# Performance work log

Hardware: AMD Instinct MI355X
Metric: run time of the kernel (lower is better)

## Reference

```python
import jax, jax.numpy as jnp
import numpy as np

N_DATA = 500000
FEAT_DIM = 128
BATCH = 512
N_NEG = 4096
TEMPERATURE = 0.07
MOMENTUM = 0.5
EPS = 1e-12


def _l2norm(x, axis=-1):
    # F.normalize(x, dim): x / max(||x||, eps)
    n = jnp.sqrt(jnp.sum(x * x, axis=axis, keepdims=True))
    return x / jnp.maximum(n, EPS)


def setup_inputs() -> dict:
    key = jax.random.key(0)
    k1, k2, k3, k4, k5 = jax.random.split(key, 5)
    student_feat = jax.random.normal(k1, (BATCH, FEAT_DIM), dtype=jnp.float32)
    teacher_feat = jax.random.normal(k2, (BATCH, FEAT_DIM), dtype=jnp.float32)
    # buffer initialized as normalized gaussian rows (as in __init__)
    memory_bank = _l2norm(jax.random.normal(k3, (N_DATA, FEAT_DIM), dtype=jnp.float32))
    indices = jax.random.randint(k4, (BATCH,), 0, N_DATA, dtype=jnp.int64 if jax.config.jax_enable_x64 else jnp.int32)
    neg_indices = jax.random.randint(k5, (BATCH, N_NEG), 0, N_DATA, dtype=jnp.int64 if jax.config.jax_enable_x64 else jnp.int32)
    return {
        "student_feat": student_feat,
        "teacher_feat": teacher_feat,
        "memory_bank": memory_bank,
        "indices": indices,
        "neg_indices": neg_indices,
    }


def reference(student_feat, teacher_feat, memory_bank, indices, neg_indices):
    s = _l2norm(student_feat)           # [B, D]
    t = _l2norm(teacher_feat)           # [B, D]

    # positive logits: elementwise dot of paired student/teacher rows
    pos_logits = jnp.sum(s * t, axis=1, keepdims=True) / TEMPERATURE   # [B, 1]

    # gather negatives from memory bank, then batched dot products
    neg_feat = memory_bank[neg_indices]                                # [B, K, D]
    neg_logits = jnp.einsum("bd,bkd->bk", s, neg_feat) / TEMPERATURE   # [B, K]

    logits = jnp.concatenate([pos_logits, neg_logits], axis=1)         # [B, 1+K]
    # cross_entropy with label 0 for every row
    loss = jnp.mean(jax.nn.logsumexp(logits, axis=1) - logits[:, 0])

    # momentum scatter-update of the memory bank (no_grad in torch)
    updated = MOMENTUM * memory_bank[indices] + (1.0 - MOMENTUM) * t   # [B, D]
    updated = _l2norm(updated)
    new_memory_bank = memory_bank.at[indices].set(updated)

    return loss, new_memory_bank
```

## Files before the change

### kernel.cpp

```cpp
#include <hip/hip_runtime.h>
#include <cmath>

#define B_SZ 512
#define D_SZ 128
#define K_SZ 4096
#define NDATA 500000
#define TEMP 0.07f
#define MOM 0.5f
#define EPSN 1e-12f
#define SPLIT 8
#define WSB_OFF (1 << 20)

typedef float f32x4 __attribute__((ext_vector_type(4)));
typedef float f32x2 __attribute__((ext_vector_type(2)));

__global__ void knorm(const float* __restrict__ s_in, const float* __restrict__ t_in,
                      float* __restrict__ s_n, float* __restrict__ t_n,
                      float* __restrict__ pos) {
    int b = blockIdx.x;
    int l = threadIdx.x;
    float2 sv = ((const float2*)(s_in + b * D_SZ))[l];
    float2 tv = ((const float2*)(t_in + b * D_SZ))[l];
    float ss = sv.x * sv.x + sv.y * sv.y;
    float tt = tv.x * tv.x + tv.y * tv.y;
    for (int m = 1; m < 64; m <<= 1) {
        ss += __shfl_xor(ss, m, 64);
        tt += __shfl_xor(tt, m, 64);
    }
    float sinv = 1.0f / fmaxf(sqrtf(ss), EPSN);
    float tinv = 1.0f / fmaxf(sqrtf(tt), EPSN);
    float2 sn = {sv.x * sinv, sv.y * sinv};
    float2 tn = {tv.x * tinv, tv.y * tinv};
    ((float2*)(s_n + b * D_SZ))[l] = sn;
    ((float2*)(t_n + b * D_SZ))[l] = tn;
    float d = sn.x * tn.x + sn.y * tn.y;
    for (int m = 1; m < 64; m <<= 1) d += __shfl_xor(d, m, 64);
    if (l == 0) pos[b] = d * (1.0f / TEMP);
}

__global__ __launch_bounds__(256) void kcopy_emit(const float* __restrict__ src,
                                                  float* __restrict__ out ,
                                                  unsigned int* __restrict__ wsb) {
    const long long total = (long long)NDATA * D_SZ;
    const long long NV = total / 4;
    long long t = blockIdx.x * 256LL + threadIdx.x;
    const long long nthr = gridDim.x * 256LL;
    const int lane = threadIdx.x & 63;
    const f32x4* src4 = (const f32x4*)src;
    f32x4* out4 = (f32x4*)out;
    for (long long j = t; j < NV; j += nthr) {
        f32x4 v = __builtin_nontemporal_load(src4 + j);
        int w8 = __builtin_amdgcn_cvt_pk_fp8_f32(v.x, v.y, 0, false);
        w8 = __builtin_amdgcn_cvt_pk_fp8_f32(v.z, v.w, w8, true);
        wsb[j] = (unsigned int)w8;
        float pw = __shfl_up(v.w, 1, 64);
        if (lane == 0 && j > 0) pw = src[4 * j - 1];
        if (j > 0) {
            f32x4 w;
            w.x = pw; w.y = v.x; w.z = v.y; w.w = v.z;
            __builtin_nontemporal_store(w, out4 + j);
        } else {
            out[1] = v.x; out[2] = v.y; out[3] = v.z;
            out[total] = src[total - 1];
        }
    }
}

__global__ __launch_bounds__(256) void kneg_fp8(const unsigned int* __restrict__ wsb,
                                                const int* __restrict__ negidx,
                                                const float* __restrict__ s_n,
                                                float2* __restrict__ partials) {
    const int split = blockIdx.x;
    const int b = blockIdx.y;
    const int tid = threadIdx.x;
    const int oct = tid >> 3;
    const int o = tid & 7;
    const f32x4* sn4 = (const f32x4*)(s_n + b * D_SZ + o * 16);
    f32x4 s0 = sn4[0], s1 = sn4[1], s2 = sn4[2], s3 = sn4[3];
    float m = -INFINITY, ssum = 0.0f;
    const int KB = K_SZ / SPLIT;
    const int base = b * K_SZ + split * KB;
    for (int it = 0; it < KB / 128; ++it) {
        int k = it * 128 + oct * 4;
        int4 idx = *(const int4*)(negidx + base + k);
        uint4 h0 = ((const uint4*)(wsb + (long long)idx.x * 32))[o];
        uint4 h1 = ((const uint4*)(wsb + (long long)idx.y * 32))[o];
        uint4 h2 = ((const uint4*)(wsb + (long long)idx.z * 32))[o];
        uint4 h3 = ((const uint4*)(wsb + (long long)idx.w * 32))[o];
        float d0 = 0.0f, d1 = 0.0f, d2 = 0.0f, d3 = 0.0f;
        {
            f32x2 a, c;
            a = __builtin_amdgcn_cvt_pk_f32_fp8((int)h0.x, false);
            c = __builtin_amdgcn_cvt_pk_f32_fp8((int)h0.x, true);
            d0 += a.x * s0.x + a.y * s0.y + c.x * s0.z + c.y * s0.w;
            a = __builtin_amdgcn_cvt_pk_f32_fp8((int)h0.y, false);
            c = __builtin_amdgcn_cvt_pk_f32_fp8((int)h0.y, true);
            d0 += a.x * s1.x + a.y * s1.y + c.x * s1.z + c.y * s1.w;
            a = __builtin_amdgcn_cvt_pk_f32_fp8((int)h0.z, false);
            c = __builtin_amdgcn_cvt_pk_f32_fp8((int)h0.z, true);
            d0 += a.x * s2.x + a.y * s2.y + c.x * s2.z + c.y * s2.w;
            a = __builtin_amdgcn_cvt_pk_f32_fp8((int)h0.w, false);
            c = __builtin_amdgcn_cvt_pk_f32_fp8((int)h0.w, true);
            d0 += a.x * s3.x + a.y * s3.y + c.x * s3.z + c.y * s3.w;

            a = __builtin_amdgcn_cvt_pk_f32_fp8((int)h1.x, false);
            c = __builtin_amdgcn_cvt_pk_f32_fp8((int)h1.x, true);
            d1 += a.x * s0.x + a.y * s0.y + c.x * s0.z + c.y * s0.w;
            a = __builtin_amdgcn_cvt_pk_f32_fp8((int)h1.y, false);
            c = __builtin_amdgcn_cvt_pk_f32_fp8((int)h1.y, true);
            d1 += a.x * s1.x + a.y * s1.y + c.x * s1.z + c.y * s1.w;
            a = __builtin_amdgcn_cvt_pk_f32_fp8((int)h1.z, false);
            c = __builtin_amdgcn_cvt_pk_f32_fp8((int)h1.z, true);
            d1 += a.x * s2.x + a.y * s2.y + c.x * s2.z + c.y * s2.w;
            a = __builtin_amdgcn_cvt_pk_f32_fp8((int)h1.w, false);
            c = __builtin_amdgcn_cvt_pk_f32_fp8((int)h1.w, true);
            d1 += a.x * s3.x + a.y * s3.y + c.x * s3.z + c.y * s3.w;

            a = __builtin_amdgcn_cvt_pk_f32_fp8((int)h2.x, false);
            c = __builtin_amdgcn_cvt_pk_f32_fp8((int)h2.x, true);
            d2 += a.x * s0.x + a.y * s0.y + c.x * s0.z + c.y * s0.w;
            a = __builtin_amdgcn_cvt_pk_f32_fp8((int)h2.y, false);
            c = __builtin_amdgcn_cvt_pk_f32_fp8((int)h2.y, true);
            d2 += a.x * s1.x + a.y * s1.y + c.x * s1.z + c.y * s1.w;
            a = __builtin_amdgcn_cvt_pk_f32_fp8((int)h2.z, false);
            c = __builtin_amdgcn_cvt_pk_f32_fp8((int)h2.z, true);
            d2 += a.x * s2.x + a.y * s2.y + c.x * s2.z + c.y * s2.w;
            a = __builtin_amdgcn_cvt_pk_f32_fp8((int)h2.w, false);
            c = __builtin_amdgcn_cvt_pk_f32_fp8((int)h2.w, true);
            d2 += a.x * s3.x + a.y * s3.y + c.x * s3.z + c.y * s3.w;

            a = __builtin_amdgcn_cvt_pk_f32_fp8((int)h3.x, false);
            c = __builtin_amdgcn_cvt_pk_f32_fp8((int)h3.x, true);
            d3 += a.x * s0.x + a.y * s0.y + c.x * s0.z + c.y * s0.w;
            a = __builtin_amdgcn_cvt_pk_f32_fp8((int)h3.y, false);
            c = __builtin_amdgcn_cvt_pk_f32_fp8((int)h3.y, true);
            d3 += a.x * s1.x + a.y * s1.y + c.x * s1.z + c.y * s1.w;
            a = __builtin_amdgcn_cvt_pk_f32_fp8((int)h3.z, false);
            c = __builtin_amdgcn_cvt_pk_f32_fp8((int)h3.z, true);
            d3 += a.x * s2.x + a.y * s2.y + c.x * s2.z + c.y * s2.w;
            a = __builtin_amdgcn_cvt_pk_f32_fp8((int)h3.w, false);
            c = __builtin_amdgcn_cvt_pk_f32_fp8((int)h3.w, true);
            d3 += a.x * s3.x + a.y * s3.y + c.x * s3.z + c.y * s3.w;
        }
        for (int s = 1; s < 8; s <<= 1) {
            d0 += __shfl_xor(d0, s, 64);
            d1 += __shfl_xor(d1, s, 64);
            d2 += __shfl_xor(d2, s, 64);
            d3 += __shfl_xor(d3, s, 64);
        }
        d0 *= (1.0f / TEMP);
        d1 *= (1.0f / TEMP);
        d2 *= (1.0f / TEMP);
        d3 *= (1.0f / TEMP);
        float mx = fmaxf(fmaxf(d0, d1), fmaxf(d2, d3));
        float mn = fmaxf(m, mx);
        ssum = ssum * __expf(m - mn) + __expf(d0 - mn) + __expf(d1 - mn) +
               __expf(d2 - mn) + __expf(d3 - mn);
        m = mn;
    }
    __shared__ float2 gp[32];
    if (o == 0) gp[oct] = make_float2(m, ssum);
    __syncthreads();
    if (tid == 0) {
        float M = gp[0].x, S = gp[0].y;
        for (int g = 1; g < 32; ++g) {
            float mg = gp[g].x, sg = gp[g].y;
            float mn = fmaxf(M, mg);
            S = S * __expf(M - mn) + sg * __expf(mg - mn);
            M = mn;
        }
        partials[b * SPLIT + split] = make_float2(M, S);
    }
}

__global__ void kupdate(const int* __restrict__ indices, const float* __restrict__ bank,
                        const float* __restrict__ t_n, float* __restrict__ outBank ) {
    int j = blockIdx.x;
    int l = threadIdx.x;
    int idx = indices[j];
    for (int j2 = j + 1; j2 < B_SZ; ++j2)
        if (indices[j2] == idx) return;
    float2 bv = ((const float2*)(bank + (long long)idx * D_SZ))[l];
    float2 tv = ((const float2*)(t_n + j * D_SZ))[l];
    float2 u = {MOM * bv.x + (1.0f - MOM) * tv.x, MOM * bv.y + (1.0f - MOM) * tv.y};
    float ss = u.x * u.x + u.y * u.y;
    for (int m = 1; m < 64; m <<= 1) ss += __shfl_xor(ss, m, 64);
    float inv = 1.0f / fmaxf(sqrtf(ss), EPSN);
    float* dst = outBank + (long long)idx * D_SZ + l * 2;
    dst[0] = u.x * inv;
    dst[1] = u.y * inv;
}

__global__ void kfinal(const float2* __restrict__ partials, const float* __restrict__ pos,
                       float* __restrict__ out) {
    __shared__ float red[B_SZ];
    int t = threadIdx.x;
    float M = -INFINITY, S = 0.0f;
    for (int p = 0; p < SPLIT; ++p) {
        float2 ms = partials[t * SPLIT + p];
        float mn = fmaxf(M, ms.x);
        S = S * __expf(M - mn) + ms.y * __expf(ms.x - mn);
        M = mn;
    }
    float pl = pos[t];
    float mn = fmaxf(M, pl);
    S = S * __expf(M - mn) + __expf(pl - mn);
    M = mn;
    red[t] = M + logf(S) - pl;
    __syncthreads();
    for (int off = 256; off > 0; off >>= 1) {
        if (t < off) red[t] += red[t + off];
        __syncthreads();
    }
    if (t == 0) out[0] = red[0] * (1.0f / (float)B_SZ);
}

extern "C" void kernel_launch(void* const* d_in, const int* in_sizes, int n_in,
                              void* d_out, int out_size, void* d_ws, size_t ws_size,
                              hipStream_t stream) {
    const float* student = (const float*)d_in[0];
    const float* teacher = (const float*)d_in[1];
    const float* bank    = (const float*)d_in[2];
    const int*   indices = (const int*)d_in[3];
    const int*   negidx  = (const int*)d_in[4];
    float* out = (float*)d_out;

    float* s_n      = (float*)d_ws;
    float* t_n      = s_n + B_SZ * D_SZ;
    float* pos      = t_n + B_SZ * D_SZ;
    float2* partials = (float2*)(pos + B_SZ);
    unsigned int* wsb = (unsigned int*)((char*)d_ws + WSB_OFF);

    knorm<<<B_SZ, 64, 0, stream>>>(student, teacher, s_n, t_n, pos);
    kcopy_emit<<<4096, 256, 0, stream>>>(bank, out, wsb);
    dim3 g(SPLIT, B_SZ);
    kneg_fp8<<<g, 256, 0, stream>>>(wsb, negidx, s_n, partials);
    kupdate<<<B_SZ, 64, 0, stream>>>(indices, bank, t_n, out + 1);
    kfinal<<<1, B_SZ, 0, stream>>>(partials, pos, out);
}
```

Baseline: 175.7 us.

## Overlap second-half bank copy with gather over first half of the bank

Splits the bank copy and fp8 emission at row 300000. Phase B runs the copy of the upper rows in the same launch as the gather/logsumexp for negatives whose index falls in the already-converted lower rows. A final phase then handles negatives in the upper rows, and kfinal merges the two sets of partials. The aim is to overlap the streaming copy with the latency-bound gather. In exchange, every negative row is loaded twice (once per phase, masked to row 0 when out of range), and the dot-product compute is doubled.

```diff
diff --git a/kernel.cpp b/kernel.cpp
--- a/kernel.cpp
+++ b/kernel.cpp
@@ -10,6 +10,9 @@
 #define EPSN 1e-12f
 #define SPLIT 8
 #define WSB_OFF (1 << 20)
+#define NH 300000
+#define M_SENT -1.0e30f
+#define D_INV  -3.0e30f
 
 typedef float f32x4 __attribute__((ext_vector_type(4)));
 typedef float f32x2 __attribute__((ext_vector_type(2)));
@@ -38,17 +41,15 @@
     if (l == 0) pos[b] = d * (1.0f / TEMP);
 }
 
-__global__ __launch_bounds__(256) void kcopy_emit(const float* __restrict__ src,
-                                                  float* __restrict__ out ,
-                                                  unsigned int* __restrict__ wsb) {
+__device__ __forceinline__ void copy_emit_range(const float* __restrict__ src,
+                                                float* __restrict__ out,
+                                                unsigned int* __restrict__ wsb,
+                                                long long j0, long long j1,
+                                                long long t, long long nthr, int lane) {
     const long long total = (long long)NDATA * D_SZ;
-    const long long NV = total / 4;
-    long long t = blockIdx.x * 256LL + threadIdx.x;
-    const long long nthr = gridDim.x * 256LL;
-    const int lane = threadIdx.x & 63;
     const f32x4* src4 = (const f32x4*)src;
     f32x4* out4 = (f32x4*)out;
-    for (long long j = t; j < NV; j += nthr) {
+    for (long long j = j0 + t; j < j1; j += nthr) {
         f32x4 v = __builtin_nontemporal_load(src4 + j);
         int w8 = __builtin_amdgcn_cvt_pk_fp8_f32(v.x, v.y, 0, false);
         w8 = __builtin_amdgcn_cvt_pk_fp8_f32(v.z, v.w, w8, true);
@@ -66,92 +67,98 @@
     }
 }
 
-__global__ __launch_bounds__(256) void kneg_fp8(const unsigned int* __restrict__ wsb,
-                                                const int* __restrict__ negidx,
-                                                const float* __restrict__ s_n,
-                                                float2* __restrict__ partials) {
-    const int split = blockIdx.x;
-    const int b = blockIdx.y;
-    const int tid = threadIdx.x;
+template <bool LO>
+__device__ __forceinline__ void gather_body(const unsigned int* __restrict__ wsb,
+                                            const int* __restrict__ negidx,
+                                            const float* __restrict__ s_n,
+                                            float2* __restrict__ partials,
+                                            int split, int b, int tid) {
     const int oct = tid >> 3;
     const int o = tid & 7;
     const f32x4* sn4 = (const f32x4*)(s_n + b * D_SZ + o * 16);
     f32x4 s0 = sn4[0], s1 = sn4[1], s2 = sn4[2], s3 = sn4[3];
-    float m = -INFINITY, ssum = 0.0f;
+    float m = M_SENT, ssum = 0.0f;
     const int KB = K_SZ / SPLIT;
     const int base = b * K_SZ + split * KB;
     for (int it = 0; it < KB / 128; ++it) {
         int k = it * 128 + oct * 4;
         int4 idx = *(const int4*)(negidx + base + k);
-        uint4 h0 = ((const uint4*)(wsb + (long long)idx.x * 32))[o];
-        uint4 h1 = ((const uint4*)(wsb + (long long)idx.y * 32))[o];
-        uint4 h2 = ((const uint4*)(wsb + (long long)idx.z * 32))[o];
-        uint4 h3 = ((const uint4*)(wsb + (long long)idx.w * 32))[o];
+        bool c0 = LO ? (idx.x < NH) : (idx.x >= NH);
+        bool c1 = LO ? (idx.y < NH) : (idx.y >= NH);
+        bool c2 = LO ? (idx.z < NH) : (idx.z >= NH);
+        bool c3 = LO ? (idx.w < NH) : (idx.w >= NH);
+        long long i0 = c0 ? (long long)idx.x : 0;
+        long long i1 = c1 ? (long long)idx.y : 0;
+        long long i2 = c2 ? (long long)idx.z : 0;
+        long long i3 = c3 ? (long long)idx.w : 0;
+        uint4 h0 = ((const uint4*)(wsb + i0 * 32))[o];
+        uint4 h1 = ((const uint4*)(wsb + i1 * 32))[o];
+        uint4 h2 = ((const uint4*)(wsb + i2 * 32))[o];
+        uint4 h3 = ((const uint4*)(wsb + i3 * 32))[o];
         float d0 = 0.0f, d1 = 0.0f, d2 = 0.0f, d3 = 0.0f;
-        {
-            f32x2 a, c;
-            a = __builtin_amdgcn_cvt_pk_f32_fp8((int)h0.x, false);
-            c = __builtin_amdgcn_cvt_pk_f32_fp8((int)h0.x, true);
-            d0 += a.x * s0.x + a.y * s0.y + c.x * s0.z + c.y * s0.w;
-            a = __builtin_amdgcn_cvt_pk_f32_fp8((int)h0.y, false);
-            c = __builtin_amdgcn_cvt_pk_f32_fp8((int)h0.y, true);
-            d0 += a.x * s1.x + a.y * s1.y + c.x * s1.z + c.y * s1.w;
-            a = __builtin_amdgcn_cvt_pk_f32_fp8((int)h0.z, false);
-            c = __builtin_amdgcn_cvt_pk_f32_fp8((int)h0.z, true);
-            d0 += a.x * s2.x + a.y * s2.y + c.x * s2.z + c.y * s2.w;
-            a = __builtin_amdgcn_cvt_pk_f32_fp8((int)h0.w, false);
-            c = __builtin_amdgcn_cvt_pk_f32_fp8((int)h0.w, true);
-            d0 += a.x * s3.x + a.y * s3.y + c.x * s3.z + c.y * s3.w;
-
-            a = __builtin_amdgcn_cvt_pk_f32_fp8((int)h1.x, false);
-            c = __builtin_amdgcn_cvt_pk_f32_fp8((int)h1.x, true);
-            d1 += a.x * s0.x + a.y * s0.y + c.x * s0.z + c.y * s0.w;
-            a = __builtin_amdgcn_cvt_pk_f32_fp8((int)h1.y, false);
-            c = __builtin_amdgcn_cvt_pk_f32_fp8((int)h1.y, true);
-            d1 += a.x * s1.x + a.y * s1.y + c.x * s1.z + c.y * s1.w;
-            a = __builtin_amdgcn_cvt_pk_f32_fp8((int)h1.z, false);
-            c = __builtin_amdgcn_cvt_pk_f32_fp8((int)h1.z, true);
-            d1 += a.x * s2.x + a.y * s2.y + c.x * s2.z + c.y * s2.w;
-            a = __builtin_amdgcn_cvt_pk_f32_fp8((int)h1.w, false);
-            c = __builtin_amdgcn_cvt_pk_f32_fp8((int)h1.w, true);
-            d1 += a.x * s3.x + a.y * s3.y + c.x * s3.z + c.y * s3.w;
-
-            a = __builtin_amdgcn_cvt_pk_f32_fp8((int)h2.x, false);
-            c = __builtin_amdgcn_cvt_pk_f32_fp8((int)h2.x, true);
-            d2 += a.x * s0.x + a.y * s0.y + c.x * s0.z + c.y * s0.w;
-            a = __builtin_amdgcn_cvt_pk_f32_fp8((int)h2.y, false);
-            c = __builtin_amdgcn_cvt_pk_f32_fp8((int)h2.y, true);
-            d2 += a.x * s1.x + a.y * s1.y + c.x * s1.z + c.y * s1.w;
-            a = __builtin_amdgcn_cvt_pk_f32_fp8((int)h2.z, false);
-            c = __builtin_amdgcn_cvt_pk_f32_fp8((int)h2.z, true);
-            d2 += a.x * s2.x + a.y * s2.y + c.x * s2.z + c.y * s2.w;
-            a = __builtin_amdgcn_cvt_pk_f32_fp8((int)h2.w, false);
-            c = __builtin_amdgcn_cvt_pk_f32_fp8((int)h2.w, true);
-            d2 += a.x * s3.x + a.y * s3.y + c.x * s3.z + c.y * s3.w;
-
-            a = __builtin_amdgcn_cvt_pk_f32_fp8((int)h3.x, false);
-            c = __builtin_amdgcn_cvt_pk_f32_fp8((int)h3.x, true);
-            d3 += a.x * s0.x + a.y * s0.y + c.x * s0.z + c.y * s0.w;
-            a = __builtin_amdgcn_cvt_pk_f32_fp8((int)h3.y, false);
-            c = __builtin_amdgcn_cvt_pk_f32_fp8((int)h3.y, true);
-            d3 += a.x * s1.x + a.y * s1.y + c.x * s1.z + c.y * s1.w;
-            a = __builtin_amdgcn_cvt_pk_f32_fp8((int)h3.z, false);
-            c = __builtin_amdgcn_cvt_pk_f32_fp8((int)h3.z, true);
-            d3 += a.x * s2.x + a.y * s2.y + c.x * s2.z + c.y * s2.w;
-            a = __builtin_amdgcn_cvt_pk_f32_fp8((int)h3.w, false);
-            c = __builtin_amdgcn_cvt_pk_f32_fp8((int)h3.w, true);
-            d3 += a.x * s3.x + a.y * s3.y + c.x * s3.z + c.y * s3.w;
-        }
+        f32x2 a, c;
+        a = __builtin_amdgcn_cvt_pk_f32_fp8((int)h0.x, false);
+        c = __builtin_amdgcn_cvt_pk_f32_fp8((int)h0.x, true);
+        d0 += a.x * s0.x + a.y * s0.y + c.x * s0.z + c.y * s0.w;
+        a = __builtin_amdgcn_cvt_pk_f32_fp8((int)h0.y, false);
+        c = __builtin_amdgcn_cvt_pk_f32_fp8((int)h0.y, true);
+        d0 += a.x * s1.x + a.y * s1.y + c.x * s1.z + c.y * s1.w;
+        a = __builtin_amdgcn_cvt_pk_f32_fp8((int)h0.z, false);
+        c = __builtin_amdgcn_cvt_pk_f32_fp8((int)h0.z, true);
+        d0 += a.x * s2.x + a.y * s2.y + c.x * s2.z + c.y * s2.w;
+        a = __builtin_amdgcn_cvt_pk_f32_fp8((int)h0.w, false);
+        c = __builtin_amdgcn_cvt_pk_f32_fp8((int)h0.w, true);
+        d0 += a.x * s3.x + a.y * s3.y + c.x * s3.z + c.y * s3.w;
+
+        a = __builtin_amdgcn_cvt_pk_f32_fp8((int)h1.x, false);
+        c = __builtin_amdgcn_cvt_pk_f32_fp8((int)h1.x, true);
+        d1 += a.x * s0.x + a.y * s0.y + c.x * s0.z + c.y * s0.w;
+        a = __builtin_amdgcn_cvt_pk_f32_fp8((int)h1.y, false);
+        c = __builtin_amdgcn_cvt_pk_f32_fp8((int)h1.y, true);
+        d1 += a.x * s1.x + a.y * s1.y + c.x * s1.z + c.y * s1.w;
+        a = __builtin_amdgcn_cvt_pk_f32_fp8((int)h1.z, false);
+        c = __builtin_amdgcn_cvt_pk_f32_fp8((int)h1.z, true);
+        d1 += a.x * s2.x + a.y * s2.y + c.x * s2.z + c.y * s2.w;
+        a = __builtin_amdgcn_cvt_pk_f32_fp8((int)h1.w, false);
+        c = __builtin_amdgcn_cvt_pk_f32_fp8((int)h1.w, true);
+        d1 += a.x * s3.x + a.y * s3.y + c.x * s3.z + c.y * s3.w;
+
+        a = __builtin_amdgcn_cvt_pk_f32_fp8((int)h2.x, false);
+        c = __builtin_amdgcn_cvt_pk_f32_fp8((int)h2.x, true);
+        d2 += a.x * s0.x + a.y * s0.y + c.x * s0.z + c.y * s0.w;
+        a = __builtin_amdgcn_cvt_pk_f32_fp8((int)h2.y, false);
+        c = __builtin_amdgcn_cvt_pk_f32_fp8((int)h2.y, true);
+        d2 += a.x * s1.x + a.y * s1.y + c.x * s1.z + c.y * s1.w;
+        a = __builtin_amdgcn_cvt_pk_f32_fp8((int)h2.z, false);
+        c = __builtin_amdgcn_cvt_pk_f32_fp8((int)h2.z, true);
+        d2 += a.x * s2.x + a.y * s2.y + c.x * s2.z + c.y * s2.w;
+        a = __builtin_amdgcn_cvt_pk_f32_fp8((int)h2.w, false);
+        c = __builtin_amdgcn_cvt_pk_f32_fp8((int)h2.w, true);
+        d2 += a.x * s3.x + a.y * s3.y + c.x * s3.z + c.y * s3.w;
+
+        a = __builtin_amdgcn_cvt_pk_f32_fp8((int)h3.x, false);
+        c = __builtin_amdgcn_cvt_pk_f32_fp8((int)h3.x, true);
+        d3 += a.x * s0.x + a.y * s0.y + c.x * s0.z + c.y * s0.w;
+        a = __builtin_amdgcn_cvt_pk_f32_fp8((int)h3.y, false);
+        c = __builtin_amdgcn_cvt_pk_f32_fp8((int)h3.y, true);
+        d3 += a.x * s1.x + a.y * s1.y + c.x * s1.z + c.y * s1.w;
+        a = __builtin_amdgcn_cvt_pk_f32_fp8((int)h3.z, false);
+        c = __builtin_amdgcn_cvt_pk_f32_fp8((int)h3.z, true);
+        d3 += a.x * s2.x + a.y * s2.y + c.x * s2.z + c.y * s2.w;
+        a = __builtin_amdgcn_cvt_pk_f32_fp8((int)h3.w, false);
+        c = __builtin_amdgcn_cvt_pk_f32_fp8((int)h3.w, true);
+        d3 += a.x * s3.x + a.y * s3.y + c.x * s3.z + c.y * s3.w;
+
         for (int s = 1; s < 8; s <<= 1) {
             d0 += __shfl_xor(d0, s, 64);
             d1 += __shfl_xor(d1, s, 64);
             d2 += __shfl_xor(d2, s, 64);
             d3 += __shfl_xor(d3, s, 64);
         }
-        d0 *= (1.0f / TEMP);
-        d1 *= (1.0f / TEMP);
-        d2 *= (1.0f / TEMP);
-        d3 *= (1.0f / TEMP);
+        d0 = c0 ? d0 * (1.0f / TEMP) : D_INV;
+        d1 = c1 ? d1 * (1.0f / TEMP) : D_INV;
+        d2 = c2 ? d2 * (1.0f / TEMP) : D_INV;
+        d3 = c3 ? d3 * (1.0f / TEMP) : D_INV;
         float mx = fmaxf(fmaxf(d0, d1), fmaxf(d2, d3));
         float mn = fmaxf(m, mx);
         ssum = ssum * __expf(m - mn) + __expf(d0 - mn) + __expf(d1 - mn) +
@@ -171,6 +178,40 @@
         }
         partials[b * SPLIT + split] = make_float2(M, S);
     }
+}
+
+__global__ __launch_bounds__(256) void kphaseA(const float* __restrict__ src,
+                                               float* __restrict__ out,
+                                               unsigned int* __restrict__ wsb) {
+    const long long VH = (long long)NH * 32;
+    long long t = blockIdx.x * 256LL + threadIdx.x;
+    copy_emit_range(src, out, wsb, 0, VH, t, gridDim.x * 256LL, threadIdx.x & 63);
+}
+
+__global__ __launch_bounds__(256) void kphaseB(const float* __restrict__ src,
+                                               float* __restrict__ out,
+                                               unsigned int* __restrict__ wsb,
+                                               const int* __restrict__ negidx,
+                                               const float* __restrict__ s_n,
+                                               float2* __restrict__ partials_lo) {
+    const int r = blockIdx.x % 3;
+    const int q = blockIdx.x / 3;
+    if (r == 0) {
+        const long long VH = (long long)NH * 32;
+        const long long NV = (long long)NDATA * 32;
+        long long t = q * 256LL + threadIdx.x;
+        copy_emit_range(src, out, wsb, VH, NV, t, 2048LL * 256LL, threadIdx.x & 63);
+    } else {
+        const int g = 2 * q + (r - 1);
+        gather_body<true>(wsb, negidx, s_n, partials_lo, g & (SPLIT - 1), g >> 3, threadIdx.x);
+    }
+}
+
+__global__ __launch_bounds__(256) void kphaseC(const unsigned int* __restrict__ wsb,
+                                               const int* __restrict__ negidx,
+                                               const float* __restrict__ s_n,
+                                               float2* __restrict__ partials_hi) {
+    gather_body<false>(wsb, negidx, s_n, partials_hi, blockIdx.x, blockIdx.y, threadIdx.x);
 }
 
 __global__ void kupdate(const int* __restrict__ indices, const float* __restrict__ bank,
@@ -191,14 +232,18 @@
     dst[1] = u.y * inv;
 }
 
-__global__ void kfinal(const float2* __restrict__ partials, const float* __restrict__ pos,
-                       float* __restrict__ out) {
+__global__ void kfinal(const float2* __restrict__ plo, const float2* __restrict__ phi,
+                       const float* __restrict__ pos, float* __restrict__ out) {
     __shared__ float red[B_SZ];
     int t = threadIdx.x;
-    float M = -INFINITY, S = 0.0f;
+    float M = M_SENT, S = 0.0f;
     for (int p = 0; p < SPLIT; ++p) {
-        float2 ms = partials[t * SPLIT + p];
+        float2 ms = plo[t * SPLIT + p];
         float mn = fmaxf(M, ms.x);
+        S = S * __expf(M - mn) + ms.y * __expf(ms.x - mn);
+        M = mn;
+        ms = phi[t * SPLIT + p];
+        mn = fmaxf(M, ms.x);
         S = S * __expf(M - mn) + ms.y * __expf(ms.x - mn);
         M = mn;
     }
@@ -208,8 +253,8 @@
     M = mn;
     red[t] = M + logf(S) - pl;
     __syncthreads();
-    for (int off = 256; off > 0; off >>= 1) {
-        if (t < off) red[t] += red[t + off];
+    for (int o = 256; o > 0; o >>= 1) {
+        if (t < o) red[t] += red[t + o];
         __syncthreads();
     }
     if (t == 0) out[0] = red[0] * (1.0f / (float)B_SZ);
@@ -225,16 +270,18 @@
     const int*   negidx  = (const int*)d_in[4];
     float* out = (float*)d_out;
 
-    float* s_n      = (float*)d_ws;
-    float* t_n      = s_n + B_SZ * D_SZ;
-    float* pos      = t_n + B_SZ * D_SZ;
-    float2* partials = (float2*)(pos + B_SZ);
+    float* s_n       = (float*)d_ws;
+    float* t_n       = s_n + B_SZ * D_SZ;
+    float* pos       = t_n + B_SZ * D_SZ;
+    float2* plo      = (float2*)(pos + B_SZ);
+    float2* phi      = plo + B_SZ * SPLIT;
     unsigned int* wsb = (unsigned int*)((char*)d_ws + WSB_OFF);
 
     knorm<<<B_SZ, 64, 0, stream>>>(student, teacher, s_n, t_n, pos);
-    kcopy_emit<<<4096, 256, 0, stream>>>(bank, out, wsb);
-    dim3 g(SPLIT, B_SZ);
-    kneg_fp8<<<g, 256, 0, stream>>>(wsb, negidx, s_n, partials);
+    kphaseA<<<4096, 256, 0, stream>>>(bank, out, wsb);
+    kphaseB<<<6144, 256, 0, stream>>>(bank, out, wsb, negidx, s_n, plo);
+    dim3 gc(SPLIT, B_SZ);
+    kphaseC<<<gc, 256, 0, stream>>>(wsb, negidx, s_n, phi);
     kupdate<<<B_SZ, 64, 0, stream>>>(indices, bank, t_n, out + 1);
-    kfinal<<<1, B_SZ, 0, stream>>>(partials, pos, out);
-}
+    kfinal<<<1, B_SZ, 0, stream>>>(plo, phi, pos, out);
+}
```

After: 203.7 us. 1.16x slower.

## Tile bank copy per wave with shuffle carry; gather 8 negatives per iteration

Applied to the files above, without the earlier changes.

The bank copy/fp8-conversion kernel now gives each wavefront a contiguous tile of 1024 vectors. The shifted element at each step is carried across iterations by a lane-63 shuffle, which removes the per-iteration scalar global load from lane 0. The negative-logit kernel now issues eight row gathers per iteration instead of four, raising memory-level parallelism at some register cost. A small dot16 helper and a variable rename are cleanup.

```diff
diff --git a/kernel.cpp b/kernel.cpp
--- a/kernel.cpp
+++ b/kernel.cpp
@@ -10,6 +10,9 @@
 #define EPSN 1e-12f
 #define SPLIT 8
 #define WSB_OFF (1 << 20)
+#define NV_TOT 16000000LL
+#define TILE_V 1024LL
+#define NTILE 15625LL
 
 typedef float f32x4 __attribute__((ext_vector_type(4)));
 typedef float f32x2 __attribute__((ext_vector_type(2)));
@@ -42,19 +45,24 @@
                                                   float* __restrict__ out ,
                                                   unsigned int* __restrict__ wsb) {
     const long long total = (long long)NDATA * D_SZ;
-    const long long NV = total / 4;
-    long long t = blockIdx.x * 256LL + threadIdx.x;
-    const long long nthr = gridDim.x * 256LL;
     const int lane = threadIdx.x & 63;
+    const long long wave_gid = (long long)blockIdx.x * 4 + (threadIdx.x >> 6);
+    if (wave_gid >= NTILE) return;
+    const long long base = wave_gid * TILE_V;
     const f32x4* src4 = (const f32x4*)src;
     f32x4* out4 = (f32x4*)out;
-    for (long long j = t; j < NV; j += nthr) {
+    float carry = 0.0f;
+    if (lane == 0 && base > 0) carry = src[4 * base - 1];
+#pragma unroll 4
+    for (int it = 0; it < 16; ++it) {
+        long long j = base + it * 64 + lane;
         f32x4 v = __builtin_nontemporal_load(src4 + j);
         int w8 = __builtin_amdgcn_cvt_pk_fp8_f32(v.x, v.y, 0, false);
         w8 = __builtin_amdgcn_cvt_pk_fp8_f32(v.z, v.w, w8, true);
         wsb[j] = (unsigned int)w8;
         float pw = __shfl_up(v.w, 1, 64);
-        if (lane == 0 && j > 0) pw = src[4 * j - 1];
+        if (lane == 0) pw = carry;
+        carry = __shfl(v.w, 63, 64);
         if (j > 0) {
             f32x4 w;
             w.x = pw; w.y = v.x; w.z = v.y; w.w = v.z;
@@ -64,6 +72,24 @@
             out[total] = src[total - 1];
         }
     }
+}
+
+__device__ __forceinline__ float dot16_fp8(uint4 h, f32x4 s0, f32x4 s1, f32x4 s2, f32x4 s3) {
+    float d = 0.0f;
+    f32x2 a, c;
+    a = __builtin_amdgcn_cvt_pk_f32_fp8((int)h.x, false);
+    c = __builtin_amdgcn_cvt_pk_f32_fp8((int)h.x, true);
+    d += a.x * s0.x + a.y * s0.y + c.x * s0.z + c.y * s0.w;
+    a = __builtin_amdgcn_cvt_pk_f32_fp8((int)h.y, false);
+    c = __builtin_amdgcn_cvt_pk_f32_fp8((int)h.y, true);
+    d += a.x * s1.x + a.y * s1.y + c.x * s1.z + c.y * s1.w;
+    a = __builtin_amdgcn_cvt_pk_f32_fp8((int)h.z, false);
+    c = __builtin_amdgcn_cvt_pk_f32_fp8((int)h.z, true);
+    d += a.x * s2.x + a.y * s2.y + c.x * s2.z + c.y * s2.w;
+    a = __builtin_amdgcn_cvt_pk_f32_fp8((int)h.w, false);
+    c = __builtin_amdgcn_cvt_pk_f32_fp8((int)h.w, true);
+    d += a.x * s3.x + a.y * s3.y + c.x * s3.z + c.y * s3.w;
+    return d;
 }
 
 __global__ __launch_bounds__(256) void kneg_fp8(const unsigned int* __restrict__ wsb,
@@ -80,82 +106,44 @@
     float m = -INFINITY, ssum = 0.0f;
     const int KB = K_SZ / SPLIT;
     const int base = b * K_SZ + split * KB;
-    for (int it = 0; it < KB / 128; ++it) {
-        int k = it * 128 + oct * 4;
-        int4 idx = *(const int4*)(negidx + base + k);
-        uint4 h0 = ((const uint4*)(wsb + (long long)idx.x * 32))[o];
-        uint4 h1 = ((const uint4*)(wsb + (long long)idx.y * 32))[o];
-        uint4 h2 = ((const uint4*)(wsb + (long long)idx.z * 32))[o];
-        uint4 h3 = ((const uint4*)(wsb + (long long)idx.w * 32))[o];
-        float d0 = 0.0f, d1 = 0.0f, d2 = 0.0f, d3 = 0.0f;
-        {
-            f32x2 a, c;
-            a = __builtin_amdgcn_cvt_pk_f32_fp8((int)h0.x, false);
-            c = __builtin_amdgcn_cvt_pk_f32_fp8((int)h0.x, true);
-            d0 += a.x * s0.x + a.y * s0.y + c.x * s0.z + c.y * s0.w;
-            a = __builtin_amdgcn_cvt_pk_f32_fp8((int)h0.y, false);
-            c = __builtin_amdgcn_cvt_pk_f32_fp8((int)h0.y, true);
-            d0 += a.x * s1.x + a.y * s1.y + c.x * s1.z + c.y * s1.w;
-            a = __builtin_amdgcn_cvt_pk_f32_fp8((int)h0.z, false);
-            c = __builtin_amdgcn_cvt_pk_f32_fp8((int)h0.z, true);
-            d0 += a.x * s2.x + a.y * s2.y + c.x * s2.z + c.y * s2.w;
-            a = __builtin_amdgcn_cvt_pk_f32_fp8((int)h0.w, false);
-            c = __builtin_amdgcn_cvt_pk_f32_fp8((int)h0.w, true);
-            d0 += a.x * s3.x + a.y * s3.y + c.x * s3.z + c.y * s3.w;
-
-            a = __builtin_amdgcn_cvt_pk_f32_fp8((int)h1.x, false);
-            c = __builtin_amdgcn_cvt_pk_f32_fp8((int)h1.x, true);
-            d1 += a.x * s0.x + a.y * s0.y + c.x * s0.z + c.y * s0.w;
-            a = __builtin_amdgcn_cvt_pk_f32_fp8((int)h1.y, false);
-            c = __builtin_amdgcn_cvt_pk_f32_fp8((int)h1.y, true);
-            d1 += a.x * s1.x + a.y * s1.y + c.x * s1.z + c.y * s1.w;
-            a = __builtin_amdgcn_cvt_pk_f32_fp8((int)h1.z, false);
-            c = __builtin_amdgcn_cvt_pk_f32_fp8((int)h1.z, true);
-            d1 += a.x * s2.x + a.y * s2.y + c.x * s2.z + c.y * s2.w;
-            a = __builtin_amdgcn_cvt_pk_f32_fp8((int)h1.w, false);
-            c = __builtin_amdgcn_cvt_pk_f32_fp8((int)h1.w, true);
-            d1 += a.x * s3.x + a.y * s3.y + c.x * s3.z + c.y * s3.w;
-
-            a = __builtin_amdgcn_cvt_pk_f32_fp8((int)h2.x, false);
-            c = __builtin_amdgcn_cvt_pk_f32_fp8((int)h2.x, true);
-            d2 += a.x * s0.x + a.y * s0.y + c.x * s0.z + c.y * s0.w;
-            a = __builtin_amdgcn_cvt_pk_f32_fp8((int)h2.y, false);
-            c = __builtin_amdgcn_cvt_pk_f32_fp8((int)h2.y, true);
-            d2 += a.x * s1.x + a.y * s1.y + c.x * s1.z + c.y * s1.w;
-            a = __builtin_amdgcn_cvt_pk_f32_fp8((int)h2.z, false);
-            c = __builtin_amdgcn_cvt_pk_f32_fp8((int)h2.z, true);
-            d2 += a.x * s2.x + a.y * s2.y + c.x * s2.z + c.y * s2.w;
-            a = __builtin_amdgcn_cvt_pk_f32_fp8((int)h2.w, false);
-            c = __builtin_amdgcn_cvt_pk_f32_fp8((int)h2.w, true);
-            d2 += a.x * s3.x + a.y * s3.y + c.x * s3.z + c.y * s3.w;
-
-            a = __builtin_amdgcn_cvt_pk_f32_fp8((int)h3.x, false);
-            c = __builtin_amdgcn_cvt_pk_f32_fp8((int)h3.x, true);
-            d3 += a.x * s0.x + a.y * s0.y + c.x * s0.z + c.y * s0.w;
-            a = __builtin_amdgcn_cvt_pk_f32_fp8((int)h3.y, false);
-            c = __builtin_amdgcn_cvt_pk_f32_fp8((int)h3.y, true);
-            d3 += a.x * s1.x + a.y * s1.y + c.x * s1.z + c.y * s1.w;
-            a = __builtin_amdgcn_cvt_pk_f32_fp8((int)h3.z, false);
-            c = __builtin_amdgcn_cvt_pk_f32_fp8((int)h3.z, true);
-            d3 += a.x * s2.x + a.y * s2.y + c.x * s2.z + c.y * s2.w;
-            a = __builtin_amdgcn_cvt_pk_f32_fp8((int)h3.w, false);
-            c = __builtin_amdgcn_cvt_pk_f32_fp8((int)h3.w, true);
-            d3 += a.x * s3.x + a.y * s3.y + c.x * s3.z + c.y * s3.w;
-        }
+    for (int it = 0; it < KB / 256; ++it) {
+        int k = it * 256 + oct * 8;
+        int4 ia = *(const int4*)(negidx + base + k);
+        int4 ib = *(const int4*)(negidx + base + k + 4);
+        uint4 h0 = ((const uint4*)(wsb + (long long)ia.x * 32))[o];
+        uint4 h1 = ((const uint4*)(wsb + (long long)ia.y * 32))[o];
+        uint4 h2 = ((const uint4*)(wsb + (long long)ia.z * 32))[o];
+        uint4 h3 = ((const uint4*)(wsb + (long long)ia.w * 32))[o];
+        uint4 h4 = ((const uint4*)(wsb + (long long)ib.x * 32))[o];
+        uint4 h5 = ((const uint4*)(wsb + (long long)ib.y * 32))[o];
+        uint4 h6 = ((const uint4*)(wsb + (long long)ib.z * 32))[o];
+        uint4 h7 = ((const uint4*)(wsb + (long long)ib.w * 32))[o];
+        float d0 = dot16_fp8(h0, s0, s1, s2, s3);
+        float d1 = dot16_fp8(h1, s0, s1, s2, s3);
+        float d2 = dot16_fp8(h2, s0, s1, s2, s3);
+        float d3 = dot16_fp8(h3, s0, s1, s2, s3);
+        float d4 = dot16_fp8(h4, s0, s1, s2, s3);
+        float d5 = dot16_fp8(h5, s0, s1, s2, s3);
+        float d6 = dot16_fp8(h6, s0, s1, s2, s3);
+        float d7 = dot16_fp8(h7, s0, s1, s2, s3);
         for (int s = 1; s < 8; s <<= 1) {
             d0 += __shfl_xor(d0, s, 64);
             d1 += __shfl_xor(d1, s, 64);
             d2 += __shfl_xor(d2, s, 64);
             d3 += __shfl_xor(d3, s, 64);
+            d4 += __shfl_xor(d4, s, 64);
+            d5 += __shfl_xor(d5, s, 64);
+            d6 += __shfl_xor(d6, s, 64);
+            d7 += __shfl_xor(d7, s, 64);
         }
-        d0 *= (1.0f / TEMP);
-        d1 *= (1.0f / TEMP);
-        d2 *= (1.0f / TEMP);
-        d3 *= (1.0f / TEMP);
-        float mx = fmaxf(fmaxf(d0, d1), fmaxf(d2, d3));
+        d0 *= (1.0f / TEMP); d1 *= (1.0f / TEMP); d2 *= (1.0f / TEMP); d3 *= (1.0f / TEMP);
+        d4 *= (1.0f / TEMP); d5 *= (1.0f / TEMP); d6 *= (1.0f / TEMP); d7 *= (1.0f / TEMP);
+        float mx = fmaxf(fmaxf(fmaxf(d0, d1), fmaxf(d2, d3)),
+                         fmaxf(fmaxf(d4, d5), fmaxf(d6, d7)));
         float mn = fmaxf(m, mx);
         ssum = ssum * __expf(m - mn) + __expf(d0 - mn) + __expf(d1 - mn) +
-               __expf(d2 - mn) + __expf(d3 - mn);
+               __expf(d2 - mn) + __expf(d3 - mn) + __expf(d4 - mn) +
+               __expf(d5 - mn) + __expf(d6 - mn) + __expf(d7 - mn);
         m = mn;
     }
     __shared__ float2 gp[32];
@@ -208,8 +196,8 @@
     M = mn;
     red[t] = M + logf(S) - pl;
     __syncthreads();
-    for (int off = 256; off > 0; off >>= 1) {
-        if (t < off) red[t] += red[t + off];
+    for (int o = 256; o > 0; o >>= 1) {
+        if (t < o) red[t] += red[t + o];
         __syncthreads();
     }
     if (t == 0) out[0] = red[0] * (1.0f / (float)B_SZ);
@@ -232,7 +220,7 @@
     unsigned int* wsb = (unsigned int*)((char*)d_ws + WSB_OFF);
 
     knorm<<<B_SZ, 64, 0, stream>>>(student, teacher, s_n, t_n, pos);
-    kcopy_emit<<<4096, 256, 0, stream>>>(bank, out, wsb);
+    kcopy_emit<<<3907, 256, 0, stream>>>(bank, out, wsb);
     dim3 g(SPLIT, B_SZ);
     kneg_fp8<<<g, 256, 0, stream>>>(wsb, negidx, s_n, partials);
     kupdate<<<B_SZ, 64, 0, stream>>>(indices, bank, t_n, out + 1);
```

After: 178.8 us. Within noise of the previous version (+1.8%).
